# Performance work log

Measured on AMD Instinct MI355X. Metric: run time of the kernel, lower is better.

Reference implementation:

```python
import jax, jax.numpy as jnp
import numpy as np

T, B, E, H = 1024, 8, 1024, 16
HD = E // H                       # 64
SCALE = float(HD * 1) ** -0.5     # scaling_factor = 1


def setup_inputs() -> dict:
    key = jax.random.key(0)
    ks = jax.random.split(key, 7)
    s = 0.02
    return {
        "query": jax.random.normal(ks[0], (T, B, E), jnp.float32),
        "key_padding_mask": jax.random.bernoulli(ks[1], 0.1, (B, T)),
        "attn_bias": jax.random.normal(ks[2], (1, H, T, T), jnp.float32) * 0.1,
        "wq": jax.random.normal(ks[3], (1, E, E), jnp.float32) * s,
        "wk": jax.random.normal(ks[4], (1, E, E), jnp.float32) * s,
        "wv": jax.random.normal(ks[5], (1, E, E), jnp.float32) * s,
        "wo": jax.random.normal(ks[6], (1, E, E), jnp.float32) * s,
    }


def _group_linear(x, w):
    # x: (T, B, nb*din), w: (nb, din, dout) -> (T, B, nb*dout). nb=1 here.
    t, b, _ = x.shape
    nb, din, dout = w.shape
    y = jnp.einsum('xnd,nde->xne', x.reshape(t * b, nb, din), w)
    return y.reshape(t, b, nb * dout)


def reference(query, key_padding_mask, attn_bias, wq, wk, wv, wo):
    q = _group_linear(query, wq) * SCALE
    k = _group_linear(query, wk)
    v = _group_linear(query, wv)

    # (T, B, E) -> (B*H, T, HD), matching torch view+transpose
    def split_heads(x):
        return x.reshape(T, B * H, HD).transpose(1, 0, 2)

    q, k, v = split_heads(q), split_heads(k), split_heads(v)

    scores = jnp.einsum('bth,bsh->bts', q, k).reshape(B, H, T, T)
    scores = scores + attn_bias
    scores = jnp.where(key_padding_mask[:, None, None, :], -jnp.inf, scores)
    probs = jax.nn.softmax(scores.astype(jnp.float32), axis=-1).astype(query.dtype)

    vh = v.reshape(B, H, T, HD)  # (B*H,T,HD) -> (B,H,S,HD)
    attn = jnp.einsum('bhts,bhsd->tbhd', probs, vh).reshape(T, B, H * HD)
    return _group_linear(attn, wo)
```

## Files before the change

kernel.cpp:

```cpp
#include <hip/hip_runtime.h>


typedef __bf16 bf16x8 __attribute__((ext_vector_type(8)));
typedef float f32x4 __attribute__((ext_vector_type(4)));

#define LOG2E 1.4426950408889634f
#define QSCALE 0.18033688011112042f

static __device__ __forceinline__ unsigned short f2bf_rn(float f) {
  union { float f; unsigned u; } x;
  x.f = f;
  unsigned r = (x.u + 0x7fffu + ((x.u >> 16) & 1u)) >> 16;
  return (unsigned short)r;
}
static __device__ __forceinline__ unsigned short f2bf(float f) {
  union { float f; unsigned u; } x;
  x.f = f;
  return (unsigned short)((x.u + 0x8000u) >> 16);
}

static __device__ __forceinline__ void async_cp16(const void* g, void* l) {
  __builtin_amdgcn_global_load_lds((__attribute__((address_space(1))) void*)g,
                                   (__attribute__((address_space(3))) void*)l,
                                   16, 0, 0);
}

__global__ void k_cvt(const float* __restrict__ src, unsigned short* __restrict__ dst) {
  const int idx = blockIdx.x * 256 + threadIdx.x;
  const float4 f = ((const float4*)src)[idx];
  unsigned lo = (unsigned)f2bf_rn(f.x) | ((unsigned)f2bf_rn(f.y) << 16);
  unsigned hi = (unsigned)f2bf_rn(f.z) | ((unsigned)f2bf_rn(f.w) << 16);
  uint2 v; v.x = lo; v.y = hi;
  *(uint2*)(dst + (size_t)idx * 4) = v;
}

__global__ void k_mask(const int* __restrict__ mask, float* __restrict__ Mfg) {
  const int i = blockIdx.x * 256 + threadIdx.x;
  Mfg[i] = mask[i] ? -1e30f : 0.f;
}

__global__ void k_transw(const float* __restrict__ src, unsigned short* __restrict__ dst) {
  __shared__ float tile[32][33];
  const int bx = blockIdx.x << 5;
  const int by = blockIdx.y << 5;
  const int tx = threadIdx.x, ty = threadIdx.y;
#pragma unroll
  for (int i = 0; i < 32; i += 8)
    tile[ty + i][tx] = src[(size_t)(by + ty + i) * 1024 + bx + tx];
  __syncthreads();
#pragma unroll
  for (int i = 0; i < 32; i += 8)
    dst[(size_t)(bx + ty + i) * 1024 + by + tx] = f2bf_rn(tile[tx][ty + i]);
}

__global__ __launch_bounds__(256, 2) void k_biasT(const float* __restrict__ bias,
                                                  unsigned short* __restrict__ B2) {
  __shared__ unsigned short tile[128 * 132];
  const int tid = threadIdx.x;
  const int ss = blockIdx.x, tt = blockIdx.y, h = blockIdx.z;
  const float* src = bias + ((long)h * 1024 + tt * 128) * 1024 + ss * 128;
#pragma unroll
  for (int c = 0; c < 16; ++c) {
    int flat = c * 256 + tid;
    int row = flat >> 5, col = (flat & 31) << 2;
    float4 v = *(const float4*)(src + (long)row * 1024 + col);
    unsigned short* t4 = &tile[row * 132 + col];
    t4[0] = f2bf_rn(v.x * LOG2E); t4[1] = f2bf_rn(v.y * LOG2E);
    t4[2] = f2bf_rn(v.z * LOG2E); t4[3] = f2bf_rn(v.w * LOG2E);
  }
  __syncthreads();
  const int wid = tid >> 6, lane = tid & 63, lanelo = lane & 15, quad = lane >> 4;
  unsigned short outv[64];
#pragma unroll
  for (int mi = 0; mi < 2; ++mi)
#pragma unroll
    for (int nj = 0; nj < 8; ++nj)
#pragma unroll
      for (int r = 0; r < 4; ++r)
        outv[mi * 32 + nj * 4 + r] =
            tile[(wid * 32 + mi * 16 + quad * 4 + r) * 132 + nj * 16 + lanelo];
  unsigned short* dst = B2 + ((((long)(h * 8 + tt) * 8 + ss) * 256 + tid) << 6);
#pragma unroll
  for (int i = 0; i < 8; ++i) ((uint4*)dst)[i] = ((const uint4*)outv)[i];
}

static __device__ __forceinline__ void gemm_tile_128x128(
    const unsigned short* __restrict__ A, const unsigned short* __restrict__ Bt,
    int K, long m0, long n0,
    unsigned short* As, unsigned short* Bs, f32x4 acc[4][4]) {
  const int tid = threadIdx.x;
  const int wid = tid >> 6;
  const int lane = tid & 63;
  const int lanelo = lane & 15;
  const int quad = lane >> 4;
  const int wm = (wid >> 1) << 6;
  const int wn = (wid & 1) << 6;
  const int srow = tid >> 2;
  const int scol = (tid & 3) << 3;

  for (int k0 = 0; k0 < K; k0 += 32) {
    __syncthreads();
    {
      const unsigned short* ga0 = A + (m0 + srow) * K + k0 + scol;
      const unsigned short* ga1 = A + (m0 + srow + 64) * K + k0 + scol;
      const unsigned short* gb0 = Bt + (n0 + srow) * K + k0 + scol;
      const unsigned short* gb1 = Bt + (n0 + srow + 64) * K + k0 + scol;
      char* la = (char*)As + wid * 1024;
      char* lb = (char*)Bs + wid * 1024;
      async_cp16(ga0, la);
      async_cp16(ga1, la + 4096);
      async_cp16(gb0, lb);
      async_cp16(gb1, lb + 4096);
    }
    __syncthreads();
    bf16x8 a[4], b[4];
#pragma unroll
    for (int i = 0; i < 4; ++i) {
      a[i] = *(const bf16x8*)(As + (wm + i * 16 + lanelo) * 32 + quad * 8);
      b[i] = *(const bf16x8*)(Bs + (wn + i * 16 + lanelo) * 32 + quad * 8);
    }
#pragma unroll
    for (int i = 0; i < 4; ++i)
#pragma unroll
      for (int j = 0; j < 4; ++j)
        acc[i][j] = __builtin_amdgcn_mfma_f32_16x16x32_bf16(a[i], b[j], acc[i][j], 0, 0, 0);
  }
}

__global__ __launch_bounds__(256, 2) void k_gemm_qkv(
    const unsigned short* __restrict__ A, const unsigned short* __restrict__ Bt,
    unsigned short* __restrict__ Qh, unsigned short* __restrict__ Kh,
    unsigned short* __restrict__ Vt) {
  __shared__ unsigned short smem[9216];
  unsigned short* As = smem;
  unsigned short* Bs = smem + 4096;
  f32x4 acc[4][4];
  const f32x4 z4 = {0.f, 0.f, 0.f, 0.f};
#pragma unroll
  for (int i = 0; i < 4; ++i)
#pragma unroll
    for (int j = 0; j < 4; ++j) acc[i][j] = z4;

  const long m0 = (long)blockIdx.y * 128;
  const long n0 = (long)blockIdx.x * 128;
  gemm_tile_128x128(A, Bt, 1024, m0, n0, As, Bs, acc);

  const int tid = threadIdx.x;
  const int wid = tid >> 6;
  const int lane = tid & 63;
  const int lanelo = lane & 15;
  const int quad = lane >> 4;
  const int wm = (wid >> 1) << 6;
  const int wn = (wid & 1) << 6;
  const int which = (int)(blockIdx.x >> 3);

  if (which == 2) {
    unsigned short* Vt_s = smem;
    const long t0g = m0 >> 3;
#pragma unroll
    for (int half = 0; half < 2; ++half) {
      __syncthreads();
      if ((wid & 1) == half) {
#pragma unroll
        for (int mi = 0; mi < 4; ++mi)
#pragma unroll
          for (int nj = 0; nj < 4; ++nj)
#pragma unroll
            for (int r = 0; r < 4; ++r)
              Vt_s[(wm + mi * 16 + quad * 4 + r) * 72 + nj * 16 + lanelo] =
                  f2bf(acc[mi][nj][r]);
      }
      __syncthreads();
      const int h = (((int)(n0 & 1023)) >> 6) + half;
#pragma unroll
      for (int pp = 0; pp < 2; ++pp) {
        int p = tid + pp * 256;
        int b = p >> 6, d = p & 63;
        long off = ((long)(b * 16 + h)) << 16;
        __attribute__((aligned(16))) unsigned short vals[16];
#pragma unroll
        for (int t = 0; t < 16; ++t) vals[t] = Vt_s[(t * 8 + b) * 72 + d];
        uint4* dst = (uint4*)(Vt + off + (long)d * 1024 + t0g);
        dst[0] = ((const uint4*)vals)[0];
        dst[1] = ((const uint4*)vals)[1];
      }
    }
  } else {
#pragma unroll
    for (int mi = 0; mi < 4; ++mi)
#pragma unroll
      for (int nj = 0; nj < 4; ++nj)
#pragma unroll
        for (int r = 0; r < 4; ++r) {
          int m = (int)m0 + wm + mi * 16 + quad * 4 + r;
          int n = (int)n0 + wn + nj * 16 + lanelo;
          float v = acc[mi][nj][r];
          int t = m >> 3, b = m & 7;
          int e = n & 1023, h = e >> 6, d = e & 63;
          long off = ((long)(b * 16 + h)) << 16;
          if (which == 0)
            Qh[off + t * 64 + d] = f2bf(v * QSCALE);
          else
            Kh[off + t * 64 + d] = f2bf(v);
        }
  }
}

__global__ __launch_bounds__(512, 4) void k_attn(
    const unsigned short* __restrict__ Qh, const unsigned short* __restrict__ Kh,
    const unsigned short* __restrict__ Vt, const unsigned short* __restrict__ B2,
    const float* __restrict__ Mfg, unsigned short* __restrict__ A2) {
  __shared__ unsigned short Ks[128 * 72];
  __shared__ unsigned short Vs[64 * 136];
  __shared__ unsigned short Ps[128 * 72];

  const int tid = threadIdx.x;
  const int wid = tid >> 6;
  const int lane = tid & 63;
  const int lanelo = lane & 15;
  const int quad = lane >> 4;
  const int bh = blockIdx.x;
  const int b = bh >> 4, h = bh & 15;
  const int tt = blockIdx.y;
  const int t0 = tt * 128;
  const long head = (long)bh << 16;

  bf16x8 aq[2];
#pragma unroll
  for (int ks = 0; ks < 2; ++ks)
    aq[ks] = *(const bf16x8*)(Qh + head +
                              (long)(t0 + wid * 16 + lanelo) * 64 +
                              ks * 32 + quad * 8);

  const f32x4 z4 = {0.f, 0.f, 0.f, 0.f};
  f32x4 Oacc[4];
#pragma unroll
  for (int dj = 0; dj < 4; ++dj) Oacc[dj] = z4;
  float mrow[4], lrow[4];
#pragma unroll
  for (int r = 0; r < 4; ++r) { mrow[r] = -1e30f; lrow[r] = 0.f; }

  const long biasbase = (((long)(h * 8 + tt) * 8) * 256 + (wid >> 1) * 64 + lane) * 64 +
                        (wid & 1) * 32;

  for (int s0 = 0; s0 < 1024; s0 += 128) {
    bf16x8 bfr[4];
    {
      const bf16x8* bp8 = (const bf16x8*)(B2 + biasbase + ((long)(s0 >> 7) * 256 << 6));
#pragma unroll
      for (int i = 0; i < 4; ++i) bfr[i] = bp8[i];
    }
    float madd[8];
#pragma unroll
    for (int nj = 0; nj < 8; ++nj)
      madd[nj] = Mfg[(long)b * 1024 + s0 + nj * 16 + lanelo];

    __syncthreads();
#pragma unroll
    for (int c = 0; c < 2; ++c) {
      int flat = c * 4096 + tid * 8;
      int row = flat >> 6, col = flat & 63;
      uint4 v = *(const uint4*)(Kh + head + (long)(s0 + row) * 64 + col);
      *(uint4*)&Ks[row * 72 + col] = v;
    }
#pragma unroll
    for (int c = 0; c < 2; ++c) {
      int flat = c * 4096 + tid * 8;
      int row = flat >> 7, col = flat & 127;
      uint4 v = *(const uint4*)(Vt + head + (long)row * 1024 + s0 + col);
      *(uint4*)&Vs[row * 136 + col] = v;
    }
    __syncthreads();

    f32x4 S[8];
#pragma unroll
    for (int nj = 0; nj < 8; ++nj)
#pragma unroll
      for (int r = 0; r < 4; ++r)
        S[nj][r] = (float)bfr[nj >> 1][(nj & 1) * 4 + r] + madd[nj];

#pragma unroll
    for (int ks = 0; ks < 2; ++ks) {
      bf16x8 bk[8];
#pragma unroll
      for (int nj = 0; nj < 8; ++nj)
        bk[nj] = *(const bf16x8*)(Ks + (nj * 16 + lanelo) * 72 + ks * 32 + quad * 8);
#pragma unroll
      for (int nj = 0; nj < 8; ++nj)
        S[nj] = __builtin_amdgcn_mfma_f32_16x16x32_bf16(aq[ks], bk[nj], S[nj], 0, 0, 0);
    }

#pragma unroll
    for (int r = 0; r < 4; ++r) {
      float mx = S[0][r];
#pragma unroll
      for (int nj = 1; nj < 8; ++nj) mx = fmaxf(mx, S[nj][r]);
      mx = fmaxf(mx, __shfl_xor(mx, 1, 16));
      mx = fmaxf(mx, __shfl_xor(mx, 2, 16));
      mx = fmaxf(mx, __shfl_xor(mx, 4, 16));
      mx = fmaxf(mx, __shfl_xor(mx, 8, 16));
      float mold = mrow[r];
      float mnew = fmaxf(mold, mx);
      float al = exp2f(mold - mnew);
      mrow[r] = mnew;
      float rs = 0.f;
#pragma unroll
      for (int nj = 0; nj < 8; ++nj) {
        float p = exp2f(S[nj][r] - mnew);
        S[nj][r] = p;
        rs += p;
      }
      rs += __shfl_xor(rs, 1, 16);
      rs += __shfl_xor(rs, 2, 16);
      rs += __shfl_xor(rs, 4, 16);
      rs += __shfl_xor(rs, 8, 16);
      lrow[r] = lrow[r] * al + rs;
#pragma unroll
      for (int dj = 0; dj < 4; ++dj) Oacc[dj][r] *= al;
    }

#pragma unroll
    for (int half = 0; half < 2; ++half) {
#pragma unroll
      for (int njl = 0; njl < 4; ++njl)
#pragma unroll
        for (int r = 0; r < 4; ++r)
          Ps[(wid * 16 + quad * 4 + r) * 72 + njl * 16 + lanelo] =
              f2bf(S[half * 4 + njl][r]);
#pragma unroll
      for (int ks2 = 0; ks2 < 2; ++ks2) {
        const int ks = half * 2 + ks2;
        bf16x8 ap, bv[4];
        ap = *(const bf16x8*)(Ps + (wid * 16 + lanelo) * 72 + ks2 * 32 + quad * 8);
#pragma unroll
        for (int dj = 0; dj < 4; ++dj)
          bv[dj] = *(const bf16x8*)(Vs + (dj * 16 + lanelo) * 136 + ks * 32 + quad * 8);
#pragma unroll
        for (int dj = 0; dj < 4; ++dj)
          Oacc[dj] = __builtin_amdgcn_mfma_f32_16x16x32_bf16(ap, bv[dj], Oacc[dj], 0, 0, 0);
      }
    }
  }

#pragma unroll
  for (int r = 0; r < 4; ++r) {
    float rinv = __builtin_amdgcn_rcpf(lrow[r]);
    int t = t0 + wid * 16 + quad * 4 + r;
#pragma unroll
    for (int dj = 0; dj < 4; ++dj) {
      int d = dj * 16 + lanelo;
      A2[(long)(t * 8 + b) * 1024 + h * 64 + d] = f2bf(Oacc[dj][r] * rinv);
    }
  }
}

__global__ __launch_bounds__(256, 2) void k_gemm_out(
    const unsigned short* __restrict__ A, const unsigned short* __restrict__ Bt,
    float* __restrict__ out) {
  __shared__ unsigned short As[128 * 32];
  __shared__ unsigned short Bs[128 * 32];
  f32x4 acc[4][4];
  const f32x4 z4 = {0.f, 0.f, 0.f, 0.f};
#pragma unroll
  for (int i = 0; i < 4; ++i)
#pragma unroll
    for (int j = 0; j < 4; ++j) acc[i][j] = z4;

  const long m0 = (long)blockIdx.y * 128;
  const long n0 = (long)blockIdx.x * 128;
  gemm_tile_128x128(A, Bt, 1024, m0, n0, As, Bs, acc);

  const int tid = threadIdx.x;
  const int wid = tid >> 6;
  const int lane = tid & 63;
  const int lanelo = lane & 15;
  const int quad = lane >> 4;
  const int wm = (wid >> 1) << 6;
  const int wn = (wid & 1) << 6;
#pragma unroll
  for (int mi = 0; mi < 4; ++mi)
#pragma unroll
    for (int nj = 0; nj < 4; ++nj)
#pragma unroll
      for (int r = 0; r < 4; ++r) {
        long m = m0 + wm + mi * 16 + quad * 4 + r;
        long n = n0 + wn + nj * 16 + lanelo;
        out[m * 1024 + n] = acc[mi][nj][r];
      }
}

extern "C" void kernel_launch(void* const* d_in, const int* in_sizes, int n_in,
                              void* d_out, int out_size, void* d_ws, size_t ws_size,
                              hipStream_t stream) {
  const float* query = (const float*)d_in[0];
  const int* mask = (const int*)d_in[1];
  const float* bias = (const float*)d_in[2];
  const float* wq = (const float*)d_in[3];
  const float* wk = (const float*)d_in[4];
  const float* wv = (const float*)d_in[5];
  const float* wo = (const float*)d_in[6];
  float* out = (float*)d_out;

  char* ws = (char*)d_ws;
  const size_t MB = 1024 * 1024;
  unsigned short* Abuf  = (unsigned short*)(ws);
  unsigned short* WqkvT = (unsigned short*)(ws + 16 * MB);
  unsigned short* WoT   = (unsigned short*)(ws + 22 * MB);
  unsigned short* Qh    = (unsigned short*)(ws + 24 * MB);
  unsigned short* Kh    = (unsigned short*)(ws + 40 * MB);
  unsigned short* Vt    = (unsigned short*)(ws + 56 * MB);
  unsigned short* A2    = (unsigned short*)(ws + 72 * MB);
  unsigned short* B2    = (unsigned short*)(ws + 88 * MB);
  float*          Mfg   = (float*)(ws + 120 * MB);

  k_cvt<<<dim3(8192), dim3(256), 0, stream>>>(query, Abuf);
  k_mask<<<dim3(32), dim3(256), 0, stream>>>(mask, Mfg);
  dim3 tb(32, 8);
  k_transw<<<dim3(32, 32), tb, 0, stream>>>(wq, WqkvT);
  k_transw<<<dim3(32, 32), tb, 0, stream>>>(wk, WqkvT + 1024 * 1024);
  k_transw<<<dim3(32, 32), tb, 0, stream>>>(wv, WqkvT + 2 * 1024 * 1024);
  k_transw<<<dim3(32, 32), tb, 0, stream>>>(wo, WoT);
  k_biasT<<<dim3(8, 8, 16), dim3(256), 0, stream>>>(bias, B2);
  k_gemm_qkv<<<dim3(24, 64), dim3(256), 0, stream>>>(Abuf, WqkvT, Qh, Kh, Vt);
  k_attn<<<dim3(128, 8), dim3(512), 0, stream>>>(Qh, Kh, Vt, B2, Mfg, A2);
  k_gemm_out<<<dim3(8, 64), dim3(256), 0, stream>>>(A2, WoT, out);
}
```

Before: 381.8 us.

## Merge weight transposes, swizzle GEMM block order, defer softmax row-sum reduction

Folds the four weight-transpose launches into one kernel that picks its source matrix from blockIdx.z, saving three launches. Remaps the block index in both GEMMs so that consecutive workgroups are spread across the grid, likely to spread them over the XCDs for better L2 locality. In attention, the per-tile cross-lane row-sum shuffles are removed: each lane keeps a partial running sum, and the sums are reduced once in the epilogue. The max reduction is also rewritten as a tree to shorten the dependency chain.

After: 388.1 us. No clear change (+1.6%).

```diff
diff --git a/kernel.cpp b/kernel.cpp
--- a/kernel.cpp
+++ b/kernel.cpp
@@ -39,8 +39,14 @@
   Mfg[i] = mask[i] ? -1e30f : 0.f;
 }
 
-__global__ void k_transw(const float* __restrict__ src, unsigned short* __restrict__ dst) {
+__global__ void k_transw4(const float* __restrict__ wq, const float* __restrict__ wk,
+                          const float* __restrict__ wv, const float* __restrict__ wo,
+                          unsigned short* __restrict__ d_qkv,
+                          unsigned short* __restrict__ d_o) {
   __shared__ float tile[32][33];
+  const int z = blockIdx.z;
+  const float* src = (z == 0) ? wq : (z == 1) ? wk : (z == 2) ? wv : wo;
+  unsigned short* dst = (z < 3) ? d_qkv + (size_t)z * 1024 * 1024 : d_o;
   const int bx = blockIdx.x << 5;
   const int by = blockIdx.y << 5;
   const int tx = threadIdx.x, ty = threadIdx.y;
@@ -141,8 +147,11 @@
 #pragma unroll
     for (int j = 0; j < 4; ++j) acc[i][j] = z4;
 
-  const long m0 = (long)blockIdx.y * 128;
-  const long n0 = (long)blockIdx.x * 128;
+  const int flat = blockIdx.y * 24 + blockIdx.x;
+  const int swz = (flat & 7) * 192 + (flat >> 3);
+  const int bx = swz % 24, by = swz / 24;
+  const long m0 = (long)by * 128;
+  const long n0 = (long)bx * 128;
   gemm_tile_128x128(A, Bt, 1024, m0, n0, As, Bs, acc);
 
   const int tid = threadIdx.x;
@@ -152,7 +161,7 @@
   const int quad = lane >> 4;
   const int wm = (wid >> 1) << 6;
   const int wn = (wid & 1) << 6;
-  const int which = (int)(blockIdx.x >> 3);
+  const int which = bx >> 3;
 
   if (which == 2) {
     unsigned short* Vt_s = smem;
@@ -292,9 +301,11 @@
 
 #pragma unroll
     for (int r = 0; r < 4; ++r) {
-      float mx = S[0][r];
-#pragma unroll
-      for (int nj = 1; nj < 8; ++nj) mx = fmaxf(mx, S[nj][r]);
+      float m01 = fmaxf(S[0][r], S[1][r]);
+      float m23 = fmaxf(S[2][r], S[3][r]);
+      float m45 = fmaxf(S[4][r], S[5][r]);
+      float m67 = fmaxf(S[6][r], S[7][r]);
+      float mx = fmaxf(fmaxf(m01, m23), fmaxf(m45, m67));
       mx = fmaxf(mx, __shfl_xor(mx, 1, 16));
       mx = fmaxf(mx, __shfl_xor(mx, 2, 16));
       mx = fmaxf(mx, __shfl_xor(mx, 4, 16));
@@ -310,10 +321,6 @@
         S[nj][r] = p;
         rs += p;
       }
-      rs += __shfl_xor(rs, 1, 16);
-      rs += __shfl_xor(rs, 2, 16);
-      rs += __shfl_xor(rs, 4, 16);
-      rs += __shfl_xor(rs, 8, 16);
       lrow[r] = lrow[r] * al + rs;
 #pragma unroll
       for (int dj = 0; dj < 4; ++dj) Oacc[dj][r] *= al;
@@ -344,7 +351,12 @@
 
 #pragma unroll
   for (int r = 0; r < 4; ++r) {
-    float rinv = __builtin_amdgcn_rcpf(lrow[r]);
+    float l = lrow[r];
+    l += __shfl_xor(l, 1, 16);
+    l += __shfl_xor(l, 2, 16);
+    l += __shfl_xor(l, 4, 16);
+    l += __shfl_xor(l, 8, 16);
+    float rinv = __builtin_amdgcn_rcpf(l);
     int t = t0 + wid * 16 + quad * 4 + r;
 #pragma unroll
     for (int dj = 0; dj < 4; ++dj) {
@@ -366,8 +378,10 @@
 #pragma unroll
     for (int j = 0; j < 4; ++j) acc[i][j] = z4;
 
-  const long m0 = (long)blockIdx.y * 128;
-  const long n0 = (long)blockIdx.x * 128;
+  const int flat = blockIdx.y * 8 + blockIdx.x;
+  const int swz = (flat & 7) * 64 + (flat >> 3);
+  const long m0 = (long)(swz / 8) * 128;
+  const long n0 = (long)(swz % 8) * 128;
   gemm_tile_128x128(A, Bt, 1024, m0, n0, As, Bs, acc);
 
   const int tid = threadIdx.x;
@@ -416,10 +430,7 @@
   k_cvt<<<dim3(8192), dim3(256), 0, stream>>>(query, Abuf);
   k_mask<<<dim3(32), dim3(256), 0, stream>>>(mask, Mfg);
   dim3 tb(32, 8);
-  k_transw<<<dim3(32, 32), tb, 0, stream>>>(wq, WqkvT);
-  k_transw<<<dim3(32, 32), tb, 0, stream>>>(wk, WqkvT + 1024 * 1024);
-  k_transw<<<dim3(32, 32), tb, 0, stream>>>(wv, WqkvT + 2 * 1024 * 1024);
-  k_transw<<<dim3(32, 32), tb, 0, stream>>>(wo, WoT);
+  k_transw4<<<dim3(32, 32, 4), tb, 0, stream>>>(wq, wk, wv, wo, WqkvT, WoT);
   k_biasT<<<dim3(8, 8, 16), dim3(256), 0, stream>>>(bias, B2);
   k_gemm_qkv<<<dim3(24, 64), dim3(256), 0, stream>>>(Abuf, WqkvT, Qh, Kh, Vt);
   k_attn<<<dim3(128, 8), dim3(512), 0, stream>>>(Qh, Kh, Vt, B2, Mfg, A2);
```
